# Kernel optimization log

Measured on AMD Instinct MI355X. Metric: run time of the kernel, lower is better.

The kernel has to match this reference:

```python
import jax, jax.numpy as jnp
import numpy as np

EPS = 1e-5

def _bn(x, gamma, beta):
    # BatchNorm1d forward (batch statistics, biased variance) over node dim
    mu = x.mean(axis=0)
    var = x.var(axis=0)
    return gamma * (x - mu) * jax.lax.rsqrt(var + EPS) + beta

def _gcn_conv(x, W, b, src, dst, n):
    # PyG GCNConv: h = x @ W; symmetric norm with self-loops; scatter-add to dst
    h = x @ W                                   # [N, out]
    ones = jnp.ones(src.shape, dtype=h.dtype)
    deg = jax.ops.segment_sum(ones, dst, num_segments=n) + 1.0  # +1 self-loop
    dinv = jax.lax.rsqrt(deg)                   # deg >= 1 always
    norm = dinv[src] * dinv[dst]                # [E]
    agg = jax.ops.segment_sum(h[src] * norm[:, None], dst, num_segments=n)
    agg = agg + h * (dinv * dinv)[:, None]      # self-loop contribution
    return agg + b

def setup_inputs() -> dict:
    key = jax.random.key(0)
    ks = jax.random.split(key, 10)
    N, E = 100000, 1600000
    Din, Dh, Dout = 256, 128, 128
    e_prev = jax.random.normal(ks[0], (N, Din), dtype=jnp.float32)
    edge_index = jax.random.randint(ks[1], (2, E), 0, N, dtype=jnp.int64)
    proj_W = jax.random.normal(ks[2], (Din, Din), dtype=jnp.float32) * 0.02
    proj_b = jnp.zeros((Din,), dtype=jnp.float32)
    W1 = jax.random.normal(ks[3], (Din, Dh), dtype=jnp.float32) * 0.05
    b1 = jnp.zeros((Dh,), dtype=jnp.float32)
    gamma1 = jnp.ones((Dh,), dtype=jnp.float32)
    beta1 = jnp.zeros((Dh,), dtype=jnp.float32)
    W2 = jax.random.normal(ks[4], (Dh, Dout), dtype=jnp.float32) * 0.05
    b2 = jnp.zeros((Dout,), dtype=jnp.float32)
    gamma2 = jnp.ones((Dout,), dtype=jnp.float32)
    beta2 = jnp.zeros((Dout,), dtype=jnp.float32)
    return {"e_prev": e_prev, "edge_index": edge_index,
            "proj_W": proj_W, "proj_b": proj_b,
            "W1": W1, "b1": b1, "gamma1": gamma1, "beta1": beta1,
            "W2": W2, "b2": b2, "gamma2": gamma2, "beta2": beta2}

def reference(e_prev, edge_index, proj_W, proj_b, W1, b1, gamma1, beta1, W2, b2, gamma2, beta2):
    n = e_prev.shape[0]
    src, dst = edge_index[0], edge_index[1]
    # input_projection (input_dim != hidden_dim branch)
    x = e_prev @ proj_W + proj_b
    x = _gcn_conv(x, W1, b1, src, dst, n)
    x = _bn(x, gamma1, beta1)
    x = jax.nn.relu(x)
    # dropout(0.2) is identity in eval mode
    x = _gcn_conv(x, W2, b2, src, dst, n)
    x = _bn(x, gamma2, beta2)
    return x
```

## Files before the change

kernel.cpp:

```cpp
#include <hip/hip_runtime.h>
#include <hip/hip_bf16.h>
#include <math.h>

#define BN_EPS 1e-5f
#define CAP 6144
#define MAXB 512

typedef __attribute__((ext_vector_type(8))) short short8;
typedef __attribute__((ext_vector_type(4))) float floatx4;
typedef __attribute__((ext_vector_type(2))) unsigned uvec2;

__device__ inline float4 ntload4(const float* p) {
    floatx4 v = __builtin_nontemporal_load((const floatx4*)p);
    return make_float4(v.x, v.y, v.z, v.w);
}

__global__ void init_kernel(int* __restrict__ bcursor, int nb) {
    int i = threadIdx.x + blockIdx.x * blockDim.x;
    if (i < nb) bcursor[i] = i * CAP;
}

__global__ __launch_bounds__(256) void bucket_kernel(
    const int* __restrict__ src, const int* __restrict__ dst,
    int* __restrict__ bcursor, unsigned* __restrict__ buck, int E, int nb)
{
    __shared__ int h[MAXB], resv[MAXB], cur[MAXB];
    for (int t = threadIdx.x; t < nb; t += 256) { h[t] = 0; cur[t] = 0; }
    __syncthreads();
    int per = (E + gridDim.x - 1) / gridDim.x;
    int e0 = blockIdx.x * per;
    int e1 = min(e0 + per, E);
    for (int e = e0 + threadIdx.x; e < e1; e += 256) {
        int d = __builtin_nontemporal_load(&dst[e]);
        atomicAdd(&h[d >> 8], 1);
    }
    __syncthreads();
    for (int t = threadIdx.x; t < nb; t += 256) {
        int c = h[t];
        if (c > 0) resv[t] = atomicAdd(&bcursor[t], c);
    }
    __syncthreads();
    for (int e = e0 + threadIdx.x; e < e1; e += 256) {
        int d = __builtin_nontemporal_load(&dst[e]);
        int s = __builtin_nontemporal_load(&src[e]);
        int b = d >> 8;
        int pos = resv[b] + atomicAdd(&cur[b], 1);
        buck[pos] = ((unsigned)(d & 255) << 17) | (unsigned)s;
    }
}

__global__ __launch_bounds__(512) void scanB_kernel(
    const int* __restrict__ bcursor, int* __restrict__ csrBase, int nb)
{
    __shared__ int sc[512];
    int t = threadIdx.x;
    int v = (t < nb) ? (bcursor[t] - t * CAP) : 0;
    sc[t] = v;
    __syncthreads();
    for (int off = 1; off < 512; off <<= 1) {
        int x = (t >= off) ? sc[t - off] : 0;
        __syncthreads();
        sc[t] += x;
        __syncthreads();
    }
    if (t < nb) csrBase[t] = sc[t] - v;
    if (t == nb) csrBase[nb] = sc[nb - 1 < 0 ? 0 : nb - 1];
    if (t == 511 && nb <= 511) csrBase[nb] = sc[nb - 1];
}

__global__ __launch_bounds__(256) void csr_kernel(
    const unsigned* __restrict__ buck, const int* __restrict__ bcursor,
    const int* __restrict__ csrBase,
    int* __restrict__ cnt, int* __restrict__ rowptr, float* __restrict__ dinv,
    int* __restrict__ ssrc, int N)
{
    __shared__ int h[256], sc[256], lcur[256];
    int b = blockIdx.x;
    int t = threadIdx.x;
    h[t] = 0;
    __syncthreads();
    int base = b * CAP;
    int nB = bcursor[b] - base;
    for (int i = t; i < nB; i += 256) {
        unsigned v = __builtin_nontemporal_load(&buck[base + i]);
        atomicAdd(&h[v >> 17], 1);
    }
    __syncthreads();
    int myc = h[t];
    sc[t] = myc;
    __syncthreads();
    for (int off = 1; off < 256; off <<= 1) {
        int x = (t >= off) ? sc[t - off] : 0;
        __syncthreads();
        sc[t] += x;
        __syncthreads();
    }
    int ex = sc[t] - myc;
    lcur[t] = ex;
    int node = b * 256 + t;
    int cb = csrBase[b];
    if (node < N) {
        cnt[node]    = myc;
        rowptr[node] = cb + ex;
        dinv[node]   = rsqrtf((float)myc + 1.0f);
    }
    __syncthreads();
    for (int i = t; i < nB; i += 256) {
        unsigned v = __builtin_nontemporal_load(&buck[base + i]);
        int dloc = v >> 17;
        int pos = cb + atomicAdd(&lcur[dloc], 1);
        ssrc[pos] = (int)(v & 0x1FFFFu);
    }
}

__global__ void wcpack_kernel(const float* __restrict__ PW, const float* __restrict__ W1,
                              const float* __restrict__ pb,
                              __hip_bfloat16* __restrict__ Wf1, float* __restrict__ bc) {
    int c = threadIdx.x;
    if (blockIdx.x == 256) {
        float acc = 0.f;
        for (int k = 0; k < 256; ++k) acc = fmaf(pb[k], W1[k * 128 + c], acc);
        bc[c] = acc;
        return;
    }
    int k = blockIdx.x;
    float acc = 0.f;
    for (int kk = 0; kk < 256; ++kk) acc = fmaf(PW[k * 256 + kk], W1[kk * 128 + c], acc);
    int kc = k >> 5, r5 = k & 31, qq = r5 >> 3, j = r5 & 7;
    int ct = c >> 4, l16 = c & 15;
    int lane = qq * 16 + l16;
    Wf1[(((kc * 8 + ct) * 64) + lane) * 8 + j] = __float2bfloat16(acc);
}

template <int K>
__global__ void packW_kernel(const float* __restrict__ W, __hip_bfloat16* __restrict__ Wf) {
    int t = blockIdx.x * 256 + threadIdx.x;
    if (t >= (K / 32) * 8 * 64 * 8) return;
    int j    = t & 7;
    int lane = (t >> 3) & 63;
    int ct   = (t >> 9) & 7;
    int kc   = t >> 12;
    int k = kc * 32 + ((lane >> 4) & 3) * 8 + j;
    int c = ct * 16 + (lane & 15);
    Wf[t] = __float2bfloat16(W[k * 128 + c]);
}

__device__ inline short8 cvt8(float4 a, float4 b) {
    __hip_bfloat162 p0 = __float22bfloat162_rn(make_float2(a.x, a.y));
    __hip_bfloat162 p1 = __float22bfloat162_rn(make_float2(a.z, a.w));
    __hip_bfloat162 p2 = __float22bfloat162_rn(make_float2(b.x, b.y));
    __hip_bfloat162 p3 = __float22bfloat162_rn(make_float2(b.z, b.w));
    union { short8 s; __hip_bfloat162 h[4]; } u;
    u.h[0] = p0; u.h[1] = p1; u.h[2] = p2; u.h[3] = p3;
    return u.s;
}

template <int K, bool BN>
__global__ __launch_bounds__(256) void mfma_gemm(
    const float* __restrict__ X, const short* __restrict__ Wf,
    const float* __restrict__ bias, const float* __restrict__ dinv,
    const float* __restrict__ scale, const float* __restrict__ shift,
    __hip_bfloat16* __restrict__ Hs, int N)
{
    const int wave = threadIdx.x >> 6;
    const int lane = threadIdx.x & 63;
    const int l16  = lane & 15;
    const int q    = lane >> 4;
    const int r0   = blockIdx.x * 128 + wave * 32;

    const int ra0 = min(r0 + l16, N - 1);
    const int ra1 = min(r0 + 16 + l16, N - 1);
    const float* pA0 = X + (size_t)ra0 * K + q * 8;
    const float* pA1 = X + (size_t)ra1 * K + q * 8;
    const short8* WF = (const short8*)Wf;

    floatx4 acc[2][8];
#pragma unroll
    for (int rt = 0; rt < 2; ++rt)
#pragma unroll
        for (int ct = 0; ct < 8; ++ct) { acc[rt][ct][0] = 0.f; acc[rt][ct][1] = 0.f; acc[rt][ct][2] = 0.f; acc[rt][ct][3] = 0.f; }

#pragma unroll
    for (int kc = 0; kc < K / 32; ++kc) {
        short8 b[8];
#pragma unroll
        for (int ct = 0; ct < 8; ++ct) b[ct] = WF[(kc * 8 + ct) * 64 + lane];

        float4 x00 = ntload4(pA0 + kc * 32);
        float4 x01 = ntload4(pA0 + kc * 32 + 4);
        float4 x10 = ntload4(pA1 + kc * 32);
        float4 x11 = ntload4(pA1 + kc * 32 + 4);
        if (BN) {
            float4 sc0 = *(const float4*)(scale + kc * 32 + q * 8);
            float4 sc1 = *(const float4*)(scale + kc * 32 + q * 8 + 4);
            float4 sh0 = *(const float4*)(shift + kc * 32 + q * 8);
            float4 sh1 = *(const float4*)(shift + kc * 32 + q * 8 + 4);
            x00.x = fmaxf(fmaf(x00.x, sc0.x, sh0.x), 0.f);
            x00.y = fmaxf(fmaf(x00.y, sc0.y, sh0.y), 0.f);
            x00.z = fmaxf(fmaf(x00.z, sc0.z, sh0.z), 0.f);
            x00.w = fmaxf(fmaf(x00.w, sc0.w, sh0.w), 0.f);
            x01.x = fmaxf(fmaf(x01.x, sc1.x, sh1.x), 0.f);
            x01.y = fmaxf(fmaf(x01.y, sc1.y, sh1.y), 0.f);
            x01.z = fmaxf(fmaf(x01.z, sc1.z, sh1.z), 0.f);
            x01.w = fmaxf(fmaf(x01.w, sc1.w, sh1.w), 0.f);
            x10.x = fmaxf(fmaf(x10.x, sc0.x, sh0.x), 0.f);
            x10.y = fmaxf(fmaf(x10.y, sc0.y, sh0.y), 0.f);
            x10.z = fmaxf(fmaf(x10.z, sc0.z, sh0.z), 0.f);
            x10.w = fmaxf(fmaf(x10.w, sc0.w, sh0.w), 0.f);
            x11.x = fmaxf(fmaf(x11.x, sc1.x, sh1.x), 0.f);
            x11.y = fmaxf(fmaf(x11.y, sc1.y, sh1.y), 0.f);
            x11.z = fmaxf(fmaf(x11.z, sc1.z, sh1.z), 0.f);
            x11.w = fmaxf(fmaf(x11.w, sc1.w, sh1.w), 0.f);
        }
        short8 a0 = cvt8(x00, x01);
        short8 a1 = cvt8(x10, x11);
#pragma unroll
        for (int ct = 0; ct < 8; ++ct) {
            acc[0][ct] = __builtin_amdgcn_mfma_f32_16x16x32_bf16(a0, b[ct], acc[0][ct], 0, 0, 0);
            acc[1][ct] = __builtin_amdgcn_mfma_f32_16x16x32_bf16(a1, b[ct], acc[1][ct], 0, 0, 0);
        }
    }

    float bb[8];
#pragma unroll
    for (int ct = 0; ct < 8; ++ct) bb[ct] = bias ? bias[ct * 16 + l16] : 0.f;

#pragma unroll
    for (int rt = 0; rt < 2; ++rt) {
        int rbase = r0 + rt * 16 + q * 4;
        float dv[4];
#pragma unroll
        for (int i = 0; i < 4; ++i) dv[i] = dinv[min(rbase + i, N - 1)];
#pragma unroll
        for (int ct = 0; ct < 8; ++ct) {
#pragma unroll
            for (int i = 0; i < 4; ++i) {
                int row = rbase + i;
                if (row < N)
                    Hs[(size_t)row * 128 + ct * 16 + l16] =
                        __float2bfloat16((acc[rt][ct][i] + bb[ct]) * dv[i]);
            }
        }
    }
}

__device__ inline void acc2(uint2 u, float& x0, float& x1, float& x2, float& x3) {
    x0 += __uint_as_float(u.x << 16);
    x1 += __uint_as_float(u.x & 0xffff0000u);
    x2 += __uint_as_float(u.y << 16);
    x3 += __uint_as_float(u.y & 0xffff0000u);
}

__global__ __launch_bounds__(256) void agg_gather_kernel(
    const uint2* __restrict__ Hu, const int* __restrict__ rowptr,
    const int* __restrict__ cnt, const int* __restrict__ ssrc,
    const float* __restrict__ dinv, const float* __restrict__ bias,
    float* __restrict__ Out, int N)
{
    int node = blockIdx.x * 4 + (threadIdx.x >> 6);
    if (node >= N) return;
    int lane = threadIdx.x & 63;
    int half = lane >> 5;
    int l32  = lane & 31;
    size_t rsel = (size_t)node * 32 + l32;

    float a0 = 0.f, a1 = 0.f, a2 = 0.f, a3 = 0.f;
    float b0 = 0.f, b1 = 0.f, b2 = 0.f, b3 = 0.f;
    float c0 = 0.f, c1 = 0.f, c2 = 0.f, c3 = 0.f;
    float d0 = 0.f, d1 = 0.f, d2 = 0.f, d3 = 0.f;

    if (half == 0) acc2(Hu[rsel], a0, a1, a2, a3);

    int start = rowptr[node];
    int num   = cnt[node];
    int j = 0;
    for (; j + 8 <= num; j += 8) {
        int e = start + j + half;
        int s0 = __builtin_nontemporal_load(&ssrc[e]);
        int s1 = __builtin_nontemporal_load(&ssrc[e + 2]);
        int s2 = __builtin_nontemporal_load(&ssrc[e + 4]);
        int s3 = __builtin_nontemporal_load(&ssrc[e + 6]);
        uint2 u0 = Hu[(size_t)s0 * 32 + l32];
        uint2 u1 = Hu[(size_t)s1 * 32 + l32];
        uint2 u2 = Hu[(size_t)s2 * 32 + l32];
        uint2 u3 = Hu[(size_t)s3 * 32 + l32];
        acc2(u0, a0, a1, a2, a3);
        acc2(u1, b0, b1, b2, b3);
        acc2(u2, c0, c1, c2, c3);
        acc2(u3, d0, d1, d2, d3);
    }
    for (; j + 2 <= num; j += 2) {
        int s = __builtin_nontemporal_load(&ssrc[start + j + half]);
        acc2(Hu[(size_t)s * 32 + l32], a0, a1, a2, a3);
    }
    if (half == 0 && j < num) {
        int s = __builtin_nontemporal_load(&ssrc[start + j]);
        acc2(Hu[(size_t)s * 32 + l32], b0, b1, b2, b3);
    }

    a0 += b0 + c0 + d0;
    a1 += b1 + c1 + d1;
    a2 += b2 + c2 + d2;
    a3 += b3 + c3 + d3;
    a0 += __shfl_xor(a0, 32, 64);
    a1 += __shfl_xor(a1, 32, 64);
    a2 += __shfl_xor(a2, 32, 64);
    a3 += __shfl_xor(a3, 32, 64);

    if (half == 0) {
        float di = dinv[node];
        float4 bb = ((const float4*)bias)[l32];
        floatx4 o;
        o[0] = fmaf(a0, di, bb.x);
        o[1] = fmaf(a1, di, bb.y);
        o[2] = fmaf(a2, di, bb.z);
        o[3] = fmaf(a3, di, bb.w);
        __builtin_nontemporal_store(o, (floatx4*)Out + rsel);
    }
}

__global__ __launch_bounds__(256) void bn_stats_kernel(
    const float* __restrict__ A, float* __restrict__ partS, float* __restrict__ partQ,
    int N, int R)
{
    int col4   = threadIdx.x & 31;
    int rowoff = threadIdx.x >> 5;
    int r0 = blockIdx.x * R;
    int r1 = min(r0 + R, N);
    float4 s = make_float4(0.f, 0.f, 0.f, 0.f);
    float4 qq = make_float4(0.f, 0.f, 0.f, 0.f);
#pragma unroll 4
    for (int r = r0 + rowoff; r < r1; r += 8) {
        float4 v = *(const float4*)&A[(size_t)r * 128 + col4 * 4];
        s.x += v.x; s.y += v.y; s.z += v.z; s.w += v.w;
        qq.x = fmaf(v.x, v.x, qq.x);
        qq.y = fmaf(v.y, v.y, qq.y);
        qq.z = fmaf(v.z, v.z, qq.z);
        qq.w = fmaf(v.w, v.w, qq.w);
    }
    __shared__ float4 ls[256], lq[256];
    ls[threadIdx.x] = s;
    lq[threadIdx.x] = qq;
    __syncthreads();
    if (threadIdx.x < 32) {
        float4 ts = ls[threadIdx.x], tq = lq[threadIdx.x];
#pragma unroll
        for (int k = 1; k < 8; ++k) {
            float4 xs = ls[k * 32 + threadIdx.x];
            float4 xq = lq[k * 32 + threadIdx.x];
            ts.x += xs.x; ts.y += xs.y; ts.z += xs.z; ts.w += xs.w;
            tq.x += xq.x; tq.y += xq.y; tq.z += xq.z; tq.w += xq.w;
        }
        *(float4*)&partS[(size_t)blockIdx.x * 128 + threadIdx.x * 4] = ts;
        *(float4*)&partQ[(size_t)blockIdx.x * 128 + threadIdx.x * 4] = tq;
    }
}

__global__ void bn_final_kernel(const float* __restrict__ partS, const float* __restrict__ partQ,
                                int npart,
                                float* __restrict__ mu, float* __restrict__ rstd,
                                const float* __restrict__ gamma, const float* __restrict__ beta,
                                float* __restrict__ scale, float* __restrict__ shift, int N) {
    int c = threadIdx.x;
    if (c < 128) {
        float s = 0.f, q = 0.f;
        for (int b = 0; b < npart; ++b) {
            s += partS[(size_t)b * 128 + c];
            q += partQ[(size_t)b * 128 + c];
        }
        float m = s / (float)N;
        float v = q / (float)N - m * m;
        float rs = rsqrtf(v + BN_EPS);
        mu[c] = m;
        rstd[c] = rs;
        if (scale) {
            float sc = gamma[c] * rs;
            scale[c] = sc;
            shift[c] = fmaf(-m, sc, beta[c]);
        }
    }
}

__global__ void bn_apply_kernel(float* __restrict__ A, const float* __restrict__ gamma,
                                const float* __restrict__ beta, const float* __restrict__ mu,
                                const float* __restrict__ rstd, int N) {
    int i = blockIdx.x * blockDim.x + threadIdx.x;
    if (i >= N * 32) return;
    int c4 = i & 31;
    float4 v  = ((float4*)A)[i];
    float4 g  = ((const float4*)gamma)[c4];
    float4 b  = ((const float4*)beta)[c4];
    float4 m  = ((const float4*)mu)[c4];
    float4 rs = ((const float4*)rstd)[c4];
    floatx4 o;
    o[0] = fmaf(g.x * (v.x - m.x), rs.x, b.x);
    o[1] = fmaf(g.y * (v.y - m.y), rs.y, b.y);
    o[2] = fmaf(g.z * (v.z - m.z), rs.z, b.z);
    o[3] = fmaf(g.w * (v.w - m.w), rs.w, b.w);
    __builtin_nontemporal_store(o, (floatx4*)A + i);
}

extern "C" void kernel_launch(void* const* d_in, const int* in_sizes, int n_in,
                              void* d_out, int out_size, void* d_ws, size_t ws_size,
                              hipStream_t stream) {
    const float* e_prev = (const float*)d_in[0];
    const int*   edges  = (const int*)d_in[1];
    const float* proj_W = (const float*)d_in[2];
    const float* proj_b = (const float*)d_in[3];
    const float* W1     = (const float*)d_in[4];
    const float* b1     = (const float*)d_in[5];
    const float* gamma1 = (const float*)d_in[6];
    const float* beta1  = (const float*)d_in[7];
    const float* W2     = (const float*)d_in[8];
    const float* b2     = (const float*)d_in[9];
    const float* gamma2 = (const float*)d_in[10];
    const float* beta2  = (const float*)d_in[11];
    float* out = (float*)d_out;

    const int N = in_sizes[0] / 256;
    const int E = in_sizes[1] / 2;
    const int* src = edges;
    const int* dst = edges + E;
    const int nb = (N + 255) >> 8;
    const int R = (N + 255) / 256;

    char* p = (char*)d_ws;
    const size_t NH = (size_t)N * 128;
    __hip_bfloat16* Hs = (__hip_bfloat16*)p;  p += NH * 2;
    unsigned* buck  = (unsigned*)p; p += (size_t)nb * CAP * 4;
    int* ssrc   = (int*)p;  p += (size_t)E * 4;
    int* cnt    = (int*)p;  p += (size_t)N * 4;
    int* rowptr = (int*)p;  p += (size_t)N * 4;
    float* dinv = (float*)p; p += (size_t)N * 4;
    int* bcursor = (int*)p; p += (size_t)(nb + 16) * 4;
    int* csrBase = (int*)p; p += (size_t)(nb + 16) * 4;
    float* bc   = (float*)p; p += 128 * 4;
    float* stats = (float*)p; p += 1536 * 4;
    float* partS = (float*)p; p += 256 * 128 * 4;
    float* partQ = (float*)p; p += 256 * 128 * 4;
    __hip_bfloat16* Wf1 = (__hip_bfloat16*)p; p += 256 * 128 * 2;
    __hip_bfloat16* Wf2 = (__hip_bfloat16*)p; p += 128 * 128 * 2;
    float* mu1 = stats + 256, *rs1 = stats + 384;
    float* mu2 = stats + 768, *rs2 = stats + 896;
    float* scale1 = stats + 1024, *shift1 = stats + 1152;

    init_kernel<<<(nb + 255) / 256, 256, 0, stream>>>(bcursor, nb);
    bucket_kernel<<<512, 256, 0, stream>>>(src, dst, bcursor, buck, E, nb);
    scanB_kernel<<<1, 512, 0, stream>>>(bcursor, csrBase, nb);
    csr_kernel<<<nb, 256, 0, stream>>>(buck, bcursor, csrBase, cnt, rowptr, dinv, ssrc, N);

    wcpack_kernel<<<257, 128, 0, stream>>>(proj_W, W1, proj_b, Wf1, bc);
    packW_kernel<128><<<(128 * 128 + 255) / 256, 256, 0, stream>>>(W2, Wf2);

    const int gemm_grid = (N + 127) / 128;

    mfma_gemm<256, false><<<gemm_grid, 256, 0, stream>>>(
        e_prev, (const short*)Wf1, bc, dinv, nullptr, nullptr, Hs, N);
    agg_gather_kernel<<<(N + 3) / 4, 256, 0, stream>>>(
        (const uint2*)Hs, rowptr, cnt, ssrc, dinv, b1, out, N);
    bn_stats_kernel<<<256, 256, 0, stream>>>(out, partS, partQ, N, R);
    bn_final_kernel<<<1, 128, 0, stream>>>(partS, partQ, 256, mu1, rs1,
                                           gamma1, beta1, scale1, shift1, N);

    mfma_gemm<128, true><<<gemm_grid, 256, 0, stream>>>(
        out, (const short*)Wf2, nullptr, dinv, scale1, shift1, Hs, N);
    agg_gather_kernel<<<(N + 3) / 4, 256, 0, stream>>>(
        (const uint2*)Hs, rowptr, cnt, ssrc, dinv, b2, out, N);
    bn_stats_kernel<<<256, 256, 0, stream>>>(out, partS, partQ, N, R);
    bn_final_kernel<<<1, 128, 0, stream>>>(partS, partQ, 256, mu2, rs2,
                                           nullptr, nullptr, nullptr, nullptr, N);
    bn_apply_kernel<<<(N * 32 + 255) / 256, 256, 0, stream>>>(out, gamma2, beta2, mu2, rs2, N);
}
```

Baseline: 635.9 us.

## Merge prep kernels, fold bucket scan into CSR, widen gather to uint4 rows

Merges the weight packing, bias folding and cursor init kernels into one prep kernel. The separate bucket-prefix scan kernel is removed: each CSR block now sums the earlier bucket counts itself. The aggregation gather loads 16-byte uint4 chunks so four neighbours are fetched in parallel per wave, with a two-step shuffle reduction. Nontemporal loads and stores are replaced by plain ones. Fewer launches and wider gathers should cut overhead and latency, at the cost of redundant prefix work per CSR block and more registers in the gather.

```diff
diff --git a/kernel.cpp b/kernel.cpp
--- a/kernel.cpp
+++ b/kernel.cpp
@@ -8,16 +8,46 @@
 
 typedef __attribute__((ext_vector_type(8))) short short8;
 typedef __attribute__((ext_vector_type(4))) float floatx4;
-typedef __attribute__((ext_vector_type(2))) unsigned uvec2;
 
 __device__ inline float4 ntload4(const float* p) {
     floatx4 v = __builtin_nontemporal_load((const floatx4*)p);
     return make_float4(v.x, v.y, v.z, v.w);
 }
 
-__global__ void init_kernel(int* __restrict__ bcursor, int nb) {
-    int i = threadIdx.x + blockIdx.x * blockDim.x;
-    if (i < nb) bcursor[i] = i * CAP;
+__global__ __launch_bounds__(128) void prep_kernel(
+    const float* __restrict__ PW, const float* __restrict__ W1,
+    const float* __restrict__ pb, const float* __restrict__ W2,
+    __hip_bfloat16* __restrict__ Wf1, __hip_bfloat16* __restrict__ Wf2,
+    float* __restrict__ bc, int* __restrict__ bcursor, int nb)
+{
+    int bid = blockIdx.x;
+    int tid = threadIdx.x;
+    if (bid < 256) {
+        int k = bid, c = tid;
+        float acc = 0.f;
+        for (int kk = 0; kk < 256; ++kk) acc = fmaf(PW[k * 256 + kk], W1[kk * 128 + c], acc);
+        int kc = k >> 5, r5 = k & 31, qq = r5 >> 3, j = r5 & 7;
+        int ct = c >> 4, l16 = c & 15;
+        int lane = qq * 16 + l16;
+        Wf1[(((kc * 8 + ct) * 64) + lane) * 8 + j] = __float2bfloat16(acc);
+    } else if (bid == 256) {
+        int c = tid;
+        float acc = 0.f;
+        for (int k = 0; k < 256; ++k) acc = fmaf(pb[k], W1[k * 128 + c], acc);
+        bc[c] = acc;
+    } else if (bid < 385) {
+        int t = (bid - 257) * 128 + tid;
+        int j    = t & 7;
+        int lane = (t >> 3) & 63;
+        int ct   = (t >> 9) & 7;
+        int kc   = t >> 12;
+        int k = kc * 32 + ((lane >> 4) & 3) * 8 + j;
+        int c = ct * 16 + (lane & 15);
+        Wf2[t] = __float2bfloat16(W2[k * 128 + c]);
+    } else {
+        int i = (bid - 385) * 128 + tid;
+        if (i < nb) bcursor[i] = i * CAP;
+    }
 }
 
 __global__ __launch_bounds__(256) void bucket_kernel(
@@ -49,40 +79,29 @@
     }
 }
 
-__global__ __launch_bounds__(512) void scanB_kernel(
-    const int* __restrict__ bcursor, int* __restrict__ csrBase, int nb)
-{
-    __shared__ int sc[512];
-    int t = threadIdx.x;
-    int v = (t < nb) ? (bcursor[t] - t * CAP) : 0;
-    sc[t] = v;
-    __syncthreads();
-    for (int off = 1; off < 512; off <<= 1) {
-        int x = (t >= off) ? sc[t - off] : 0;
-        __syncthreads();
-        sc[t] += x;
-        __syncthreads();
-    }
-    if (t < nb) csrBase[t] = sc[t] - v;
-    if (t == nb) csrBase[nb] = sc[nb - 1 < 0 ? 0 : nb - 1];
-    if (t == 511 && nb <= 511) csrBase[nb] = sc[nb - 1];
-}
-
 __global__ __launch_bounds__(256) void csr_kernel(
     const unsigned* __restrict__ buck, const int* __restrict__ bcursor,
-    const int* __restrict__ csrBase,
     int* __restrict__ cnt, int* __restrict__ rowptr, float* __restrict__ dinv,
     int* __restrict__ ssrc, int N)
 {
-    __shared__ int h[256], sc[256], lcur[256];
+    __shared__ int h[256], sc[256], lcur[256], redu[256];
     int b = blockIdx.x;
     int t = threadIdx.x;
+    int part = 0;
+    for (int i = t; i < b; i += 256) part += bcursor[i] - i * CAP;
+    redu[t] = part;
     h[t] = 0;
     __syncthreads();
+    for (int off = 128; off > 0; off >>= 1) {
+        if (t < off) redu[t] += redu[t + off];
+        __syncthreads();
+    }
+    int cb = redu[0];
+
     int base = b * CAP;
     int nB = bcursor[b] - base;
     for (int i = t; i < nB; i += 256) {
-        unsigned v = __builtin_nontemporal_load(&buck[base + i]);
+        unsigned v = buck[base + i];
         atomicAdd(&h[v >> 17], 1);
     }
     __syncthreads();
@@ -98,7 +117,6 @@
     int ex = sc[t] - myc;
     lcur[t] = ex;
     int node = b * 256 + t;
-    int cb = csrBase[b];
     if (node < N) {
         cnt[node]    = myc;
         rowptr[node] = cb + ex;
@@ -106,43 +124,11 @@
     }
     __syncthreads();
     for (int i = t; i < nB; i += 256) {
-        unsigned v = __builtin_nontemporal_load(&buck[base + i]);
+        unsigned v = buck[base + i];
         int dloc = v >> 17;
         int pos = cb + atomicAdd(&lcur[dloc], 1);
         ssrc[pos] = (int)(v & 0x1FFFFu);
     }
-}
-
-__global__ void wcpack_kernel(const float* __restrict__ PW, const float* __restrict__ W1,
-                              const float* __restrict__ pb,
-                              __hip_bfloat16* __restrict__ Wf1, float* __restrict__ bc) {
-    int c = threadIdx.x;
-    if (blockIdx.x == 256) {
-        float acc = 0.f;
-        for (int k = 0; k < 256; ++k) acc = fmaf(pb[k], W1[k * 128 + c], acc);
-        bc[c] = acc;
-        return;
-    }
-    int k = blockIdx.x;
-    float acc = 0.f;
-    for (int kk = 0; kk < 256; ++kk) acc = fmaf(PW[k * 256 + kk], W1[kk * 128 + c], acc);
-    int kc = k >> 5, r5 = k & 31, qq = r5 >> 3, j = r5 & 7;
-    int ct = c >> 4, l16 = c & 15;
-    int lane = qq * 16 + l16;
-    Wf1[(((kc * 8 + ct) * 64) + lane) * 8 + j] = __float2bfloat16(acc);
-}
-
-template <int K>
-__global__ void packW_kernel(const float* __restrict__ W, __hip_bfloat16* __restrict__ Wf) {
-    int t = blockIdx.x * 256 + threadIdx.x;
-    if (t >= (K / 32) * 8 * 64 * 8) return;
-    int j    = t & 7;
-    int lane = (t >> 3) & 63;
-    int ct   = (t >> 9) & 7;
-    int kc   = t >> 12;
-    int k = kc * 32 + ((lane >> 4) & 3) * 8 + j;
-    int c = ct * 16 + (lane & 15);
-    Wf[t] = __float2bfloat16(W[k * 128 + c]);
 }
 
 __device__ inline short8 cvt8(float4 a, float4 b) {
@@ -244,15 +230,19 @@
     }
 }
 
-__device__ inline void acc2(uint2 u, float& x0, float& x1, float& x2, float& x3) {
-    x0 += __uint_as_float(u.x << 16);
-    x1 += __uint_as_float(u.x & 0xffff0000u);
-    x2 += __uint_as_float(u.y << 16);
-    x3 += __uint_as_float(u.y & 0xffff0000u);
+__device__ inline void accrow(uint4 u, float* a) {
+    a[0] += __uint_as_float(u.x << 16);
+    a[1] += __uint_as_float(u.x & 0xffff0000u);
+    a[2] += __uint_as_float(u.y << 16);
+    a[3] += __uint_as_float(u.y & 0xffff0000u);
+    a[4] += __uint_as_float(u.z << 16);
+    a[5] += __uint_as_float(u.z & 0xffff0000u);
+    a[6] += __uint_as_float(u.w << 16);
+    a[7] += __uint_as_float(u.w & 0xffff0000u);
 }
 
 __global__ __launch_bounds__(256) void agg_gather_kernel(
-    const uint2* __restrict__ Hu, const int* __restrict__ rowptr,
+    const uint4* __restrict__ Hq, const int* __restrict__ rowptr,
     const int* __restrict__ cnt, const int* __restrict__ ssrc,
     const float* __restrict__ dinv, const float* __restrict__ bias,
     float* __restrict__ Out, int N)
@@ -260,62 +250,69 @@
     int node = blockIdx.x * 4 + (threadIdx.x >> 6);
     if (node >= N) return;
     int lane = threadIdx.x & 63;
-    int half = lane >> 5;
-    int l32  = lane & 31;
-    size_t rsel = (size_t)node * 32 + l32;
-
-    float a0 = 0.f, a1 = 0.f, a2 = 0.f, a3 = 0.f;
-    float b0 = 0.f, b1 = 0.f, b2 = 0.f, b3 = 0.f;
-    float c0 = 0.f, c1 = 0.f, c2 = 0.f, c3 = 0.f;
-    float d0 = 0.f, d1 = 0.f, d2 = 0.f, d3 = 0.f;
-
-    if (half == 0) acc2(Hu[rsel], a0, a1, a2, a3);
+    int q    = lane >> 4;
+    int l16  = lane & 15;
+
+    float a0[8] = {0,0,0,0,0,0,0,0};
+    float a1[8] = {0,0,0,0,0,0,0,0};
+    float a2[8] = {0,0,0,0,0,0,0,0};
+    float a3[8] = {0,0,0,0,0,0,0,0};
+
+    if (q == 0) accrow(Hq[(size_t)node * 16 + l16], a0);
 
     int start = rowptr[node];
     int num   = cnt[node];
     int j = 0;
-    for (; j + 8 <= num; j += 8) {
-        int e = start + j + half;
-        int s0 = __builtin_nontemporal_load(&ssrc[e]);
-        int s1 = __builtin_nontemporal_load(&ssrc[e + 2]);
-        int s2 = __builtin_nontemporal_load(&ssrc[e + 4]);
-        int s3 = __builtin_nontemporal_load(&ssrc[e + 6]);
-        uint2 u0 = Hu[(size_t)s0 * 32 + l32];
-        uint2 u1 = Hu[(size_t)s1 * 32 + l32];
-        uint2 u2 = Hu[(size_t)s2 * 32 + l32];
-        uint2 u3 = Hu[(size_t)s3 * 32 + l32];
-        acc2(u0, a0, a1, a2, a3);
-        acc2(u1, b0, b1, b2, b3);
-        acc2(u2, c0, c1, c2, c3);
-        acc2(u3, d0, d1, d2, d3);
-    }
-    for (; j + 2 <= num; j += 2) {
-        int s = __builtin_nontemporal_load(&ssrc[start + j + half]);
-        acc2(Hu[(size_t)s * 32 + l32], a0, a1, a2, a3);
-    }
-    if (half == 0 && j < num) {
-        int s = __builtin_nontemporal_load(&ssrc[start + j]);
-        acc2(Hu[(size_t)s * 32 + l32], b0, b1, b2, b3);
-    }
-
-    a0 += b0 + c0 + d0;
-    a1 += b1 + c1 + d1;
-    a2 += b2 + c2 + d2;
-    a3 += b3 + c3 + d3;
-    a0 += __shfl_xor(a0, 32, 64);
-    a1 += __shfl_xor(a1, 32, 64);
-    a2 += __shfl_xor(a2, 32, 64);
-    a3 += __shfl_xor(a3, 32, 64);
-
-    if (half == 0) {
+    for (; j + 16 <= num; j += 16) {
+        int e = start + j + q;
+        int s0 = ssrc[e];
+        int s1 = ssrc[e + 4];
+        int s2 = ssrc[e + 8];
+        int s3 = ssrc[e + 12];
+        uint4 u0 = Hq[(size_t)s0 * 16 + l16];
+        uint4 u1 = Hq[(size_t)s1 * 16 + l16];
+        uint4 u2 = Hq[(size_t)s2 * 16 + l16];
+        uint4 u3 = Hq[(size_t)s3 * 16 + l16];
+        accrow(u0, a0);
+        accrow(u1, a1);
+        accrow(u2, a2);
+        accrow(u3, a3);
+    }
+    for (; j + 4 <= num; j += 4) {
+        int s = ssrc[start + j + q];
+        accrow(Hq[(size_t)s * 16 + l16], a0);
+    }
+    int rem = num - j;
+    if (q < rem) {
+        int s = ssrc[start + j + q];
+        accrow(Hq[(size_t)s * 16 + l16], a1);
+    }
+
+#pragma unroll
+    for (int i = 0; i < 8; ++i) {
+        float v = a0[i] + a1[i] + a2[i] + a3[i];
+        v += __shfl_xor(v, 16, 64);
+        v += __shfl_xor(v, 32, 64);
+        a0[i] = v;
+    }
+
+    if (q == 0) {
         float di = dinv[node];
-        float4 bb = ((const float4*)bias)[l32];
-        floatx4 o;
-        o[0] = fmaf(a0, di, bb.x);
-        o[1] = fmaf(a1, di, bb.y);
-        o[2] = fmaf(a2, di, bb.z);
-        o[3] = fmaf(a3, di, bb.w);
-        __builtin_nontemporal_store(o, (floatx4*)Out + rsel);
+        const float4* B4 = (const float4*)bias;
+        float4 bb0 = B4[l16 * 2];
+        float4 bb1 = B4[l16 * 2 + 1];
+        float4 o0, o1;
+        o0.x = fmaf(a0[0], di, bb0.x);
+        o0.y = fmaf(a0[1], di, bb0.y);
+        o0.z = fmaf(a0[2], di, bb0.z);
+        o0.w = fmaf(a0[3], di, bb0.w);
+        o1.x = fmaf(a0[4], di, bb1.x);
+        o1.y = fmaf(a0[5], di, bb1.y);
+        o1.z = fmaf(a0[6], di, bb1.z);
+        o1.w = fmaf(a0[7], di, bb1.w);
+        float4* O4 = (float4*)(Out + (size_t)node * 128 + l16 * 8);
+        O4[0] = o0;
+        O4[1] = o1;
     }
 }
 
@@ -392,12 +389,11 @@
     float4 b  = ((const float4*)beta)[c4];
     float4 m  = ((const float4*)mu)[c4];
     float4 rs = ((const float4*)rstd)[c4];
-    floatx4 o;
-    o[0] = fmaf(g.x * (v.x - m.x), rs.x, b.x);
-    o[1] = fmaf(g.y * (v.y - m.y), rs.y, b.y);
-    o[2] = fmaf(g.z * (v.z - m.z), rs.z, b.z);
-    o[3] = fmaf(g.w * (v.w - m.w), rs.w, b.w);
-    __builtin_nontemporal_store(o, (floatx4*)A + i);
+    v.x = fmaf(g.x * (v.x - m.x), rs.x, b.x);
+    v.y = fmaf(g.y * (v.y - m.y), rs.y, b.y);
+    v.z = fmaf(g.z * (v.z - m.z), rs.z, b.z);
+    v.w = fmaf(g.w * (v.w - m.w), rs.w, b.w);
+    ((float4*)A)[i] = v;
 }
 
 extern "C" void kernel_launch(void* const* d_in, const int* in_sizes, int n_in,
@@ -433,7 +429,6 @@
     int* rowptr = (int*)p;  p += (size_t)N * 4;
     float* dinv = (float*)p; p += (size_t)N * 4;
     int* bcursor = (int*)p; p += (size_t)(nb + 16) * 4;
-    int* csrBase = (int*)p; p += (size_t)(nb + 16) * 4;
     float* bc   = (float*)p; p += 128 * 4;
     float* stats = (float*)p; p += 1536 * 4;
     float* partS = (float*)p; p += 256 * 128 * 4;
@@ -444,20 +439,16 @@
     float* mu2 = stats + 768, *rs2 = stats + 896;
     float* scale1 = stats + 1024, *shift1 = stats + 1152;
 
-    init_kernel<<<(nb + 255) / 256, 256, 0, stream>>>(bcursor, nb);
+    prep_kernel<<<389, 128, 0, stream>>>(proj_W, W1, proj_b, W2, Wf1, Wf2, bc, bcursor, nb);
     bucket_kernel<<<512, 256, 0, stream>>>(src, dst, bcursor, buck, E, nb);
-    scanB_kernel<<<1, 512, 0, stream>>>(bcursor, csrBase, nb);
-    csr_kernel<<<nb, 256, 0, stream>>>(buck, bcursor, csrBase, cnt, rowptr, dinv, ssrc, N);
-
-    wcpack_kernel<<<257, 128, 0, stream>>>(proj_W, W1, proj_b, Wf1, bc);
-    packW_kernel<128><<<(128 * 128 + 255) / 256, 256, 0, stream>>>(W2, Wf2);
+    csr_kernel<<<nb, 256, 0, stream>>>(buck, bcursor, cnt, rowptr, dinv, ssrc, N);
 
     const int gemm_grid = (N + 127) / 128;
 
     mfma_gemm<256, false><<<gemm_grid, 256, 0, stream>>>(
         e_prev, (const short*)Wf1, bc, dinv, nullptr, nullptr, Hs, N);
     agg_gather_kernel<<<(N + 3) / 4, 256, 0, stream>>>(
-        (const uint2*)Hs, rowptr, cnt, ssrc, dinv, b1, out, N);
+        (const uint4*)Hs, rowptr, cnt, ssrc, dinv, b1, out, N);
     bn_stats_kernel<<<256, 256, 0, stream>>>(out, partS, partQ, N, R);
     bn_final_kernel<<<1, 128, 0, stream>>>(partS, partQ, 256, mu1, rs1,
                                            gamma1, beta1, scale1, shift1, N);
@@ -465,7 +456,7 @@
     mfma_gemm<128, true><<<gemm_grid, 256, 0, stream>>>(
         out, (const short*)Wf2, nullptr, dinv, scale1, shift1, Hs, N);
     agg_gather_kernel<<<(N + 3) / 4, 256, 0, stream>>>(
-        (const uint2*)Hs, rowptr, cnt, ssrc, dinv, b2, out, N);
+        (const uint4*)Hs, rowptr, cnt, ssrc, dinv, b2, out, N);
     bn_stats_kernel<<<256, 256, 0, stream>>>(out, partS, partQ, N, R);
     bn_final_kernel<<<1, 128, 0, stream>>>(partS, partQ, 256, mu2, rs2,
                                            nullptr, nullptr, nullptr, nullptr, N);
```

After: 609.4 us. 4.2% less time.
